# Performance work log

Measured on AMD Instinct MI355X. Metric: run time of the kernel, lower is better.

The kernel has to match this reference:

```python
import jax, jax.numpy as jnp
import numpy as np

B = 64          # graphs per batch
N_NODES = 2000  # nodes per graph (model hyperparameter: FC2 in_features)
NF = 128        # node features
H = 8           # hidden_dim
OC = 8          # out_channels
NC = 2          # n_classes
DEG = 16        # avg degree
SLOPE = 0.01


def _lin_init(key, fan_in, fan_out):
    k1, k2 = jax.random.split(key)
    s = 1.0 / np.sqrt(fan_in)
    W = jax.random.uniform(k1, (fan_in, fan_out), jnp.float32, -s, s)
    b = jax.random.uniform(k2, (fan_out,), jnp.float32, -s, s)
    return W, b


def setup_inputs() -> dict:
    key = jax.random.key(0)
    ks = jax.random.split(key, 10)
    N = B * N_NODES
    E = N * DEG
    x = jax.random.normal(ks[0], (N, NF), jnp.float32)
    # graph-local random edges, offset per graph
    local = jax.random.randint(ks[1], (2, E), 0, N_NODES)
    off = jnp.repeat(jnp.arange(B, dtype=jnp.int64) * N_NODES, E // B)
    edge_index = (local + off[None, :]).astype(jnp.int64)
    batch = jnp.repeat(jnp.arange(B, dtype=jnp.int64), N_NODES)
    W1a, b1a = _lin_init(ks[2], NF, H)
    W1b, b1b = _lin_init(ks[3], H, H)
    W2a, b2a = _lin_init(ks[4], H, H)
    W2b, b2b = _lin_init(ks[5], H, OC)
    Wf1, bf1 = _lin_init(ks[6], OC, 1)
    Wf2, bf2 = _lin_init(ks[7], N_NODES, NC)
    return {"x": x, "edge_index": edge_index, "batch": batch,
            "W1a": W1a, "b1a": b1a, "W1b": W1b, "b1b": b1b,
            "W2a": W2a, "b2a": b2a, "W2b": W2b, "b2b": b2b,
            "Wf1": Wf1, "bf1": bf1, "Wf2": Wf2, "bf2": bf2}


def _lrelu(v):
    return jnp.where(v >= 0, v, SLOPE * v)


def _gin_conv(h, src, dst, Wa, ba, Wb, bb):
    N = h.shape[0]
    agg = jax.ops.segment_sum(h[src], dst, num_segments=N)  # sum_{j->i} h_j
    z = h + agg                                             # (1+eps)*h + agg, eps=0
    z = _lrelu(z @ Wa + ba)                                 # MLP linear1 + act
    return z @ Wb + bb                                      # MLP linear2 (plain last)


def reference(x, edge_index, batch, W1a, b1a, W1b, b1b, W2a, b2a, W2b, b2b,
              Wf1, bf1, Wf2, bf2):
    src, dst = edge_index[0], edge_index[1]
    h = _gin_conv(x, src, dst, W1a, b1a, W1b, b1b)
    h = _lrelu(h)  # inter-layer activation (dropout = identity at eval)
    h = _gin_conv(h, src, dst, W2a, b2a, W2b, b2b)  # [N, OC], no act after last conv
    bsz = h.shape[0] // N_NODES
    y = h.reshape(bsz, N_NODES, OC)
    y = _lrelu(y) @ Wf1 + bf1          # FC1 -> [B, n_nodes, 1]
    y = y.reshape(bsz, N_NODES)
    y = _lrelu(y) @ Wf2 + bf2          # FC2 -> [B, n_classes]
    return jax.nn.log_softmax(y, axis=1)
```

## Files before the change

### kernel.cpp

```cpp
#include <hip/hip_runtime.h>
#include <math.h>

#define NF 128
#define HD 8
#define NPG 2000
#define EPB 8000
#define LPB 8
#define LNPB 250
#define FNPB 128
#define SLOPE 0.01f

__device__ __forceinline__ float lrelu(float v) {
    return v > 0.0f ? v : SLOPE * v;
}
__device__ __forceinline__ unsigned short f2bf(float f) {
    unsigned int u = __float_as_uint(f);
    return (unsigned short)((u + 0x7FFFu + ((u >> 16) & 1u)) >> 16);
}
__device__ __forceinline__ float bfl(unsigned int p) {
    return __uint_as_float(p << 16);
}
__device__ __forceinline__ float bfh(unsigned int p) {
    return __uint_as_float(p & 0xFFFF0000u);
}
__device__ __forceinline__ void gload_lds16(const void* g, void* l) {
    __builtin_amdgcn_global_load_lds(
        (const __attribute__((address_space(1))) unsigned int*)g,
        (__attribute__((address_space(3))) unsigned int*)l, 16, 0, 0);
}

__global__ __launch_bounds__(1024) void k_featsort(
    const float* __restrict__ x, const float* __restrict__ W1a,
    const int* __restrict__ ei, unsigned short* __restrict__ t1b,
    unsigned short* __restrict__ gcolb, int* __restrict__ rpc,
    int N, int E, int NC)
{
    __shared__ union {
        struct { float tile[FNPB * NF]; float wl[8 * 132]; } f;
        struct { int cnt[NPG]; unsigned int pck[EPB]; int srt[EPB];
                 int wtot[16]; int wpre[16]; } s;
    } sm;

    const int tid = threadIdx.x;

    if ((int)blockIdx.x < NC) {
        const int b = blockIdx.x;
        const int g = b >> 2;
        const int lane = tid & 63;
        const int wv = tid >> 6;
        const int nodeBase = g * NPG;
        const int e0 = b * EPB;

        for (int i = tid; i < NPG; i += 1024) sm.s.cnt[i] = 0;
        __syncthreads();

        for (int e = e0 + tid; e < e0 + EPB; e += 1024) {
            int src = ei[e] - nodeBase;
            int dl = ei[E + e] - nodeBase;
            sm.s.pck[e - e0] = ((unsigned int)dl << 11) | (unsigned int)src;
            atomicAdd(&sm.s.cnt[dl], 1);
        }
        __syncthreads();

        int c0 = 0, c1 = 0;
        if (tid < 1000) { c0 = sm.s.cnt[2 * tid]; c1 = sm.s.cnt[2 * tid + 1]; }
        int s = c0 + c1;
        int isc = s;
#pragma unroll
        for (int d = 1; d < 64; d <<= 1) {
            int o = __shfl_up(isc, d);
            if (lane >= d) isc += o;
        }
        if (lane == 63) sm.s.wtot[wv] = isc;
        __syncthreads();
        if (wv == 0) {
            int v = (lane < 16) ? sm.s.wtot[lane] : 0;
            int iv = v;
#pragma unroll
            for (int d = 1; d < 16; d <<= 1) {
                int o = __shfl_up(iv, d);
                if (lane >= d) iv += o;
            }
            if (lane < 16) sm.s.wpre[lane] = iv - v;
        }
        __syncthreads();
        int excl = isc - s + sm.s.wpre[wv];

        int* rpb = rpc + (size_t)b * (NPG + 1);
        if (tid < 1000) {
            sm.s.cnt[2 * tid]     = excl;
            sm.s.cnt[2 * tid + 1] = excl + c0;
            rpb[2 * tid]     = excl;
            rpb[2 * tid + 1] = excl + c0;
        }
        if (tid == 0) rpb[NPG] = EPB;
        __syncthreads();

        for (int i = tid; i < EPB; i += 1024) {
            unsigned int p = sm.s.pck[i];
            int dl = (int)(p >> 11);
            int src = (int)(p & 2047u);
            int pos = atomicAdd(&sm.s.cnt[dl], 1);
            sm.s.srt[pos] = src;
        }
        __syncthreads();

        unsigned int* dst = (unsigned int*)(gcolb + (size_t)b * EPB);
        for (int i = tid; i < EPB / 2; i += 1024) {
            unsigned int lo = (unsigned int)sm.s.srt[2 * i] & 0xFFFFu;
            unsigned int hi = (unsigned int)sm.s.srt[2 * i + 1] << 16;
            dst[i] = lo | hi;
        }
    } else {
        const size_t base = (size_t)(blockIdx.x - NC) * FNPB;
        const int lane = tid & 63;
        const int wv6 = tid >> 6;

        {
            int wcol = tid >> 7;
            int wk   = tid & 127;
            sm.f.wl[wcol * 132 + wk] = W1a[wk * 8 + wcol];
        }

        const float* xg = x + base * NF;
        char* tb = (char*)sm.f.tile;
#pragma unroll
        for (int i = 0; i < 4; ++i) {
            int s = wv6 * 256 + i * 64 + lane;
            int n = s >> 5, j = s & 31;
            gload_lds16(xg + n * NF + ((j ^ (n & 7)) << 2), tb + s * 16);
        }
        __syncthreads();

        const int col   = tid & 7;
        const int khalf = (tid >> 3) & 1;
        const int np    = tid >> 4;
        const int n0    = np * 2;
        const int ex0 = n0 & 7, ex1 = (n0 + 1) & 7;

        const float*  tf = sm.f.tile;
        const float4* w4 = (const float4*)sm.f.wl;
        float acc0 = 0.0f, acc1 = 0.0f;
#pragma unroll 4
        for (int i = 0; i < 16; ++i) {
            int k4 = khalf * 16 + i;
            float4 r0 = *(const float4*)(tf + n0 * NF + ((k4 ^ ex0) << 2));
            float4 r1 = *(const float4*)(tf + (n0 + 1) * NF + ((k4 ^ ex1) << 2));
            float4 w  = w4[col * 33 + k4];
            acc0 += r0.x * w.x + r0.y * w.y + r0.z * w.z + r0.w * w.w;
            acc1 += r1.x * w.x + r1.y * w.y + r1.z * w.z + r1.w * w.w;
        }
        acc0 += __shfl_xor(acc0, 8);
        acc1 += __shfl_xor(acc1, 8);
        if (khalf == 0) {
            t1b[(base + n0) * HD + col]     = f2bf(acc0);
            t1b[(base + n0 + 1) * HD + col] = f2bf(acc1);
        }
    }
}

#define GATHER_CHUNK(P)                                                       \
    {                                                                         \
        int b0 = rs[P], cnt = re[P] - b0;                                     \
        int sl[8];                                                            \
        _Pragma("unroll")                                                     \
        for (int j = 0; j < 8; ++j) {                                         \
            int idx = (j < cnt) ? (b0 + j) : 0;                               \
            sl[j] = colp[P][idx];                                             \
        }                                                                     \
        _Pragma("unroll")                                                     \
        for (int j = 0; j < 8; ++j) {                                         \
            float w = (j < cnt) ? 1.0f : 0.0f;                                \
            uint4 v = tbl[sl[j]];                                             \
            a0 += w * bfl(v.x); a1 += w * bfh(v.x);                           \
            a2 += w * bfl(v.y); a3 += w * bfh(v.y);                           \
            a4 += w * bfl(v.z); a5 += w * bfh(v.z);                           \
            a6 += w * bfl(v.w); a7 += w * bfh(v.w);                           \
        }                                                                     \
        for (int e2 = b0 + 8; e2 < b0 + cnt; ++e2) {                          \
            uint4 v = tbl[colp[P][e2]];                                       \
            a0 += bfl(v.x); a1 += bfh(v.x);                                   \
            a2 += bfl(v.y); a3 += bfh(v.y);                                   \
            a4 += bfl(v.z); a5 += bfh(v.z);                                   \
            a6 += bfl(v.w); a7 += bfh(v.w);                                   \
        }                                                                     \
    }

__global__ __launch_bounds__(512) void k_l1(
    const unsigned short* __restrict__ t1b, const int* __restrict__ rpc,
    const unsigned short* __restrict__ gcolb, unsigned short* __restrict__ ub,
    const float* __restrict__ b1a, const float* __restrict__ W1b,
    const float* __restrict__ b1b, const float* __restrict__ W2a)
{
    __shared__ uint4 tbl[2048];
    __shared__ float wts[144];

    const int b = blockIdx.x;
    const int g = b >> 3;
    const int q = b & 7;
    const int tid = threadIdx.x;

    if (tid < 144) {
        float v;
        if (tid < 8)       v = b1a[tid];
        else if (tid < 72) v = W1b[tid - 8];
        else if (tid < 80) v = b1b[tid - 72];
        else               v = W2a[tid - 80];
        wts[tid] = v;
    }

    {
        const uint4* src4 = (const uint4*)(t1b + (size_t)g * NPG * HD);
        const int lane = tid & 63, w8 = tid >> 6;
        char* tb = (char*)tbl;
#pragma unroll
        for (int i = 0; i < 4; ++i) {
            int s = w8 * 256 + i * 64 + lane;
            gload_lds16(src4 + s, tb + s * 16);
        }
    }
    __syncthreads();

    if (tid < 2 * LNPB) {
        const int node = tid >> 1;
        const int half = tid & 1;
        const int nl = q * LNPB + node;
        int rs[2], re[2];
        const unsigned short* colp[2];
#pragma unroll
        for (int p = 0; p < 2; ++p) {
            int ch = half * 2 + p;
            const int* rpb = rpc + (size_t)((g << 2) + ch) * (NPG + 1);
            colp[p] = gcolb + (size_t)((g << 2) + ch) * EPB;
            rs[p] = rpb[nl]; re[p] = rpb[nl + 1];
        }
        float a0 = 0, a1 = 0, a2 = 0, a3 = 0, a4 = 0, a5 = 0, a6 = 0, a7 = 0;
        GATHER_CHUNK(0) GATHER_CHUNK(1)
        a0 += __shfl_xor(a0, 1); a1 += __shfl_xor(a1, 1);
        a2 += __shfl_xor(a2, 1); a3 += __shfl_xor(a3, 1);
        a4 += __shfl_xor(a4, 1); a5 += __shfl_xor(a5, 1);
        a6 += __shfl_xor(a6, 1); a7 += __shfl_xor(a7, 1);

        if (half == 0) {
            uint4 sv = tbl[nl];
            float z[HD];
            z[0] = lrelu(bfl(sv.x) + a0 + wts[0]); z[1] = lrelu(bfh(sv.x) + a1 + wts[1]);
            z[2] = lrelu(bfl(sv.y) + a2 + wts[2]); z[3] = lrelu(bfh(sv.y) + a3 + wts[3]);
            z[4] = lrelu(bfl(sv.z) + a4 + wts[4]); z[5] = lrelu(bfh(sv.z) + a5 + wts[5]);
            z[6] = lrelu(bfl(sv.w) + a6 + wts[6]); z[7] = lrelu(bfh(sv.w) + a7 + wts[7]);

            float h[HD];
#pragma unroll
            for (int j = 0; j < HD; ++j) {
                float acc = wts[72 + j];
#pragma unroll
                for (int c = 0; c < HD; ++c) acc += z[c] * wts[8 + c * HD + j];
                h[j] = lrelu(acc);
            }
            float uu[HD];
#pragma unroll
            for (int j = 0; j < HD; ++j) {
                float acc = 0.0f;
#pragma unroll
                for (int c = 0; c < HD; ++c) acc += h[c] * wts[80 + c * HD + j];
                uu[j] = acc;
            }
            uint4 pk;
            pk.x = (unsigned int)f2bf(uu[0]) | ((unsigned int)f2bf(uu[1]) << 16);
            pk.y = (unsigned int)f2bf(uu[2]) | ((unsigned int)f2bf(uu[3]) << 16);
            pk.z = (unsigned int)f2bf(uu[4]) | ((unsigned int)f2bf(uu[5]) << 16);
            pk.w = (unsigned int)f2bf(uu[6]) | ((unsigned int)f2bf(uu[7]) << 16);
            ((uint4*)ub)[(size_t)g * NPG + nl] = pk;
        }
    }
}

__global__ __launch_bounds__(512) void k_l2(
    const unsigned short* __restrict__ ub, const int* __restrict__ rpc,
    const unsigned short* __restrict__ gcolb,
    const float* __restrict__ b2a, const float* __restrict__ W2b,
    const float* __restrict__ b2b, const float* __restrict__ Wf1,
    const float* __restrict__ bf1, const float* __restrict__ Wf2,
    float* __restrict__ bparts)
{
    __shared__ uint4 tbl[2048];
    __shared__ float wts[89];
    __shared__ float red[16];

    const int b = blockIdx.x;
    const int g = b >> 3;
    const int q = b & 7;
    const int tid = threadIdx.x;
    const int lane = tid & 63;
    const int wv = tid >> 6;

    if (tid < 89) {
        float v;
        if (tid < 8)       v = b2a[tid];
        else if (tid < 72) v = W2b[tid - 8];
        else if (tid < 80) v = b2b[tid - 72];
        else if (tid < 88) v = Wf1[tid - 80];
        else               v = bf1[0];
        wts[tid] = v;
    }

    {
        const uint4* src4 = (const uint4*)(ub + (size_t)g * NPG * HD);
        char* tb = (char*)tbl;
#pragma unroll
        for (int i = 0; i < 4; ++i) {
            int s = wv * 256 + i * 64 + lane;
            gload_lds16(src4 + s, tb + s * 16);
        }
    }
    __syncthreads();

    float acc0 = 0.0f, acc1 = 0.0f;
    if (tid < 2 * LNPB) {
        const int node = tid >> 1;
        const int half = tid & 1;
        const int nl = q * LNPB + node;
        int rs[2], re[2];
        const unsigned short* colp[2];
#pragma unroll
        for (int p = 0; p < 2; ++p) {
            int ch = half * 2 + p;
            const int* rpb = rpc + (size_t)((g << 2) + ch) * (NPG + 1);
            colp[p] = gcolb + (size_t)((g << 2) + ch) * EPB;
            rs[p] = rpb[nl]; re[p] = rpb[nl + 1];
        }
        float a0 = 0, a1 = 0, a2 = 0, a3 = 0, a4 = 0, a5 = 0, a6 = 0, a7 = 0;
        GATHER_CHUNK(0) GATHER_CHUNK(1)
        a0 += __shfl_xor(a0, 1); a1 += __shfl_xor(a1, 1);
        a2 += __shfl_xor(a2, 1); a3 += __shfl_xor(a3, 1);
        a4 += __shfl_xor(a4, 1); a5 += __shfl_xor(a5, 1);
        a6 += __shfl_xor(a6, 1); a7 += __shfl_xor(a7, 1);

        if (half == 0) {
            uint4 sv = tbl[nl];
            float z[HD];
            z[0] = lrelu(bfl(sv.x) + a0 + wts[0]); z[1] = lrelu(bfh(sv.x) + a1 + wts[1]);
            z[2] = lrelu(bfl(sv.y) + a2 + wts[2]); z[3] = lrelu(bfh(sv.y) + a3 + wts[3]);
            z[4] = lrelu(bfl(sv.z) + a4 + wts[4]); z[5] = lrelu(bfh(sv.z) + a5 + wts[5]);
            z[6] = lrelu(bfl(sv.w) + a6 + wts[6]); z[7] = lrelu(bfh(sv.w) + a7 + wts[7]);

            float svl = wts[88];
#pragma unroll
            for (int j = 0; j < HD; ++j) {
                float acc = wts[72 + j];
#pragma unroll
                for (int c = 0; c < HD; ++c) acc += z[c] * wts[8 + c * HD + j];
                svl += lrelu(acc) * wts[80 + j];
            }
            float pf = lrelu(svl);
            float2 wf = *(const float2*)(Wf2 + (size_t)nl * 2);
            acc0 = pf * wf.x;
            acc1 = pf * wf.y;
        }
    }

#pragma unroll
    for (int off = 32; off > 0; off >>= 1) {
        acc0 += __shfl_down(acc0, off);
        acc1 += __shfl_down(acc1, off);
    }
    if (lane == 0) { red[wv * 2] = acc0; red[wv * 2 + 1] = acc1; }
    __syncthreads();

    if (tid == 0) {
        float y0 = 0.f, y1 = 0.f;
#pragma unroll
        for (int w = 0; w < 8; ++w) { y0 += red[w * 2]; y1 += red[w * 2 + 1]; }
        *(float2*)(bparts + (size_t)b * 2) = make_float2(y0, y1);
    }
}

__global__ __launch_bounds__(64) void k_fin(const float* __restrict__ bparts,
                                            const float* __restrict__ bf2,
                                            float* __restrict__ out, int Bn) {
    int g = threadIdx.x;
    if (g >= Bn) return;
    float y0 = bf2[0], y1 = bf2[1];
#pragma unroll
    for (int b = 0; b < LPB; ++b) {
        float2 v = *(const float2*)(bparts + (size_t)(g * LPB + b) * 2);
        y0 += v.x; y1 += v.y;
    }
    float m = fmaxf(y0, y1);
    float lse = m + logf(expf(y0 - m) + expf(y1 - m));
    out[g * 2 + 0] = y0 - lse;
    out[g * 2 + 1] = y1 - lse;
}

extern "C" void kernel_launch(void* const* d_in, const int* in_sizes, int n_in,
                              void* d_out, int out_size, void* d_ws, size_t ws_size,
                              hipStream_t stream) {
    const float* x   = (const float*)d_in[0];
    const int*   ei  = (const int*)  d_in[1];
    const float* W1a = (const float*)d_in[3];
    const float* b1a = (const float*)d_in[4];
    const float* W1b = (const float*)d_in[5];
    const float* b1b = (const float*)d_in[6];
    const float* W2a = (const float*)d_in[7];
    const float* b2a = (const float*)d_in[8];
    const float* W2b = (const float*)d_in[9];
    const float* b2b = (const float*)d_in[10];
    const float* Wf1 = (const float*)d_in[11];
    const float* bf1 = (const float*)d_in[12];
    const float* Wf2 = (const float*)d_in[13];
    const float* bf2 = (const float*)d_in[14];

    int N   = in_sizes[0] / NF;
    int E   = in_sizes[1] / 2;
    int Bn  = N / NPG;
    int NC  = Bn * 4;

    unsigned short* t1b   = (unsigned short*)d_ws;
    unsigned short* ubuf  = t1b + (size_t)N * HD;
    unsigned short* gcolb = ubuf + (size_t)N * HD;
    int*            rpc   = (int*)(gcolb + (size_t)E);
    float*          bparts= (float*)(rpc + (size_t)NC * (NPG + 1) + 16);

    k_featsort<<<NC + N / FNPB, 1024, 0, stream>>>(x, W1a, ei, t1b, gcolb, rpc,
                                                   N, E, NC);
    k_l1 <<<Bn * LPB, 512, 0, stream>>>(t1b, rpc, gcolb, ubuf, b1a, W1b, b1b, W2a);
    k_l2 <<<Bn * LPB, 512, 0, stream>>>(ubuf, rpc, gcolb, b2a, W2b, b2b, Wf1,
                                        bf1, Wf2, bparts);
    k_fin<<<1, 64, 0, stream>>>(bparts, bf2, (float*)d_out, Bn);
}
```

Measured before the change: 157.6 us.

## Fuse GIN layer kernels and finalizer into one kernel with grid barrier

Merges the layer-1, layer-2 and final log-softmax kernels into a single kernel. A global atomic barrier separates the two layers, and a last-block-done counter runs the final reduction. Each block keeps its edge-neighbour indices and its own layer-1 output in registers, so layer 2 does not reload the CSR column indices or the self features. This removes two kernel launches and some redundant loads. In exchange it depends on all 512 blocks being co-resident for the spin barrier (hence launch_bounds 512,4) and adds register pressure.

```diff
diff --git a/kernel.cpp b/kernel.cpp
--- a/kernel.cpp
+++ b/kernel.cpp
@@ -33,7 +33,7 @@
     const float* __restrict__ x, const float* __restrict__ W1a,
     const int* __restrict__ ei, unsigned short* __restrict__ t1b,
     unsigned short* __restrict__ gcolb, int* __restrict__ rpc,
-    int N, int E, int NC)
+    int* __restrict__ bar, int N, int E, int NC)
 {
     __shared__ union {
         struct { float tile[FNPB * NF]; float wl[8 * 132]; } f;
@@ -45,6 +45,7 @@
 
     if ((int)blockIdx.x < NC) {
         const int b = blockIdx.x;
+        if (b == 0 && tid < 4) bar[tid] = 0;
         const int g = b >> 2;
         const int lane = tid & 63;
         const int wv = tid >> 6;
@@ -159,26 +160,30 @@
     }
 }
 
-#define GATHER_CHUNK(P)                                                       \
+#define LOADSL(SL, RS, RE, CP)                                                \
     {                                                                         \
-        int b0 = rs[P], cnt = re[P] - b0;                                     \
-        int sl[8];                                                            \
+        int cnt = (RE) - (RS);                                                \
         _Pragma("unroll")                                                     \
         for (int j = 0; j < 8; ++j) {                                         \
-            int idx = (j < cnt) ? (b0 + j) : 0;                               \
-            sl[j] = colp[P][idx];                                             \
+            int idx = (j < cnt) ? ((RS) + j) : 0;                             \
+            SL[j] = CP[idx];                                                  \
         }                                                                     \
+    }
+
+#define GATHER_SAVED(SL, RS, RE, CP)                                          \
+    {                                                                         \
+        int cnt = (RE) - (RS);                                                \
         _Pragma("unroll")                                                     \
         for (int j = 0; j < 8; ++j) {                                         \
             float w = (j < cnt) ? 1.0f : 0.0f;                                \
-            uint4 v = tbl[sl[j]];                                             \
+            uint4 v = tbl[SL[j]];                                             \
             a0 += w * bfl(v.x); a1 += w * bfh(v.x);                           \
             a2 += w * bfl(v.y); a3 += w * bfh(v.y);                           \
             a4 += w * bfl(v.z); a5 += w * bfh(v.z);                           \
             a6 += w * bfl(v.w); a7 += w * bfh(v.w);                           \
         }                                                                     \
-        for (int e2 = b0 + 8; e2 < b0 + cnt; ++e2) {                          \
-            uint4 v = tbl[colp[P][e2]];                                       \
+        for (int e2 = (RS) + 8; e2 < (RE); ++e2) {                            \
+            uint4 v = tbl[CP[e2]];                                            \
             a0 += bfl(v.x); a1 += bfh(v.x);                                   \
             a2 += bfl(v.y); a3 += bfh(v.y);                                   \
             a4 += bfl(v.z); a5 += bfh(v.z);                                   \
@@ -186,19 +191,29 @@
         }                                                                     \
     }
 
-__global__ __launch_bounds__(512) void k_l1(
+__global__ __launch_bounds__(512, 4) void k_l12(
     const unsigned short* __restrict__ t1b, const int* __restrict__ rpc,
     const unsigned short* __restrict__ gcolb, unsigned short* __restrict__ ub,
     const float* __restrict__ b1a, const float* __restrict__ W1b,
-    const float* __restrict__ b1b, const float* __restrict__ W2a)
+    const float* __restrict__ b1b, const float* __restrict__ W2a,
+    const float* __restrict__ b2a, const float* __restrict__ W2b,
+    const float* __restrict__ b2b, const float* __restrict__ Wf1,
+    const float* __restrict__ bf1, const float* __restrict__ Wf2,
+    const float* __restrict__ bf2, float* __restrict__ bparts,
+    int* __restrict__ bar, float* __restrict__ out)
 {
     __shared__ uint4 tbl[2048];
     __shared__ float wts[144];
+    __shared__ float wt2[89];
+    __shared__ float red[16];
+    __shared__ int lastFlag;
 
     const int b = blockIdx.x;
     const int g = b >> 3;
     const int q = b & 7;
     const int tid = threadIdx.x;
+    const int lane = tid & 63;
+    const int wv = tid >> 6;
 
     if (tid < 144) {
         float v;
@@ -208,34 +223,54 @@
         else               v = W2a[tid - 80];
         wts[tid] = v;
     }
+    {
+        int t2 = tid - 160;
+        if (t2 >= 0 && t2 < 89) {
+            float v;
+            if (t2 < 8)       v = b2a[t2];
+            else if (t2 < 72) v = W2b[t2 - 8];
+            else if (t2 < 80) v = b2b[t2 - 72];
+            else if (t2 < 88) v = Wf1[t2 - 80];
+            else              v = bf1[0];
+            wt2[t2] = v;
+        }
+    }
 
     {
         const uint4* src4 = (const uint4*)(t1b + (size_t)g * NPG * HD);
-        const int lane = tid & 63, w8 = tid >> 6;
         char* tb = (char*)tbl;
 #pragma unroll
         for (int i = 0; i < 4; ++i) {
-            int s = w8 * 256 + i * 64 + lane;
+            int s = wv * 256 + i * 64 + lane;
             gload_lds16(src4 + s, tb + s * 16);
         }
     }
     __syncthreads();
 
-    if (tid < 2 * LNPB) {
-        const int node = tid >> 1;
-        const int half = tid & 1;
-        const int nl = q * LNPB + node;
-        int rs[2], re[2];
-        const unsigned short* colp[2];
-#pragma unroll
-        for (int p = 0; p < 2; ++p) {
-            int ch = half * 2 + p;
-            const int* rpb = rpc + (size_t)((g << 2) + ch) * (NPG + 1);
-            colp[p] = gcolb + (size_t)((g << 2) + ch) * EPB;
-            rs[p] = rpb[nl]; re[p] = rpb[nl + 1];
-        }
+    const int node = tid >> 1;
+    const int half = tid & 1;
+    const int nl = q * LNPB + node;
+    const bool act = node < LNPB;
+    int rs0 = 0, re0 = 0, rs1 = 0, re1 = 0;
+    const unsigned short* cp0 = gcolb;
+    const unsigned short* cp1 = gcolb;
+    int sl0[8], sl1[8];
+    float uu0 = 0, uu1 = 0, uu2 = 0, uu3 = 0, uu4 = 0, uu5 = 0, uu6 = 0, uu7 = 0;
+
+    if (act) {
+        const int ch0 = half * 2, ch1 = half * 2 + 1;
+        const int* rp0 = rpc + (size_t)((g << 2) + ch0) * (NPG + 1);
+        const int* rp1 = rpc + (size_t)((g << 2) + ch1) * (NPG + 1);
+        cp0 = gcolb + (size_t)((g << 2) + ch0) * EPB;
+        cp1 = gcolb + (size_t)((g << 2) + ch1) * EPB;
+        rs0 = rp0[nl]; re0 = rp0[nl + 1];
+        rs1 = rp1[nl]; re1 = rp1[nl + 1];
+        LOADSL(sl0, rs0, re0, cp0)
+        LOADSL(sl1, rs1, re1, cp1)
+
         float a0 = 0, a1 = 0, a2 = 0, a3 = 0, a4 = 0, a5 = 0, a6 = 0, a7 = 0;
-        GATHER_CHUNK(0) GATHER_CHUNK(1)
+        GATHER_SAVED(sl0, rs0, re0, cp0)
+        GATHER_SAVED(sl1, rs1, re1, cp1)
         a0 += __shfl_xor(a0, 1); a1 += __shfl_xor(a1, 1);
         a2 += __shfl_xor(a2, 1); a3 += __shfl_xor(a3, 1);
         a4 += __shfl_xor(a4, 1); a5 += __shfl_xor(a5, 1);
@@ -265,6 +300,8 @@
                 for (int c = 0; c < HD; ++c) acc += h[c] * wts[80 + c * HD + j];
                 uu[j] = acc;
             }
+            uu0 = uu[0]; uu1 = uu[1]; uu2 = uu[2]; uu3 = uu[3];
+            uu4 = uu[4]; uu5 = uu[5]; uu6 = uu[6]; uu7 = uu[7];
             uint4 pk;
             pk.x = (unsigned int)f2bf(uu[0]) | ((unsigned int)f2bf(uu[1]) << 16);
             pk.y = (unsigned int)f2bf(uu[2]) | ((unsigned int)f2bf(uu[3]) << 16);
@@ -273,36 +310,23 @@
             ((uint4*)ub)[(size_t)g * NPG + nl] = pk;
         }
     }
-}
-
-__global__ __launch_bounds__(512) void k_l2(
-    const unsigned short* __restrict__ ub, const int* __restrict__ rpc,
-    const unsigned short* __restrict__ gcolb,
-    const float* __restrict__ b2a, const float* __restrict__ W2b,
-    const float* __restrict__ b2b, const float* __restrict__ Wf1,
-    const float* __restrict__ bf1, const float* __restrict__ Wf2,
-    float* __restrict__ bparts)
-{
-    __shared__ uint4 tbl[2048];
-    __shared__ float wts[89];
-    __shared__ float red[16];
-
-    const int b = blockIdx.x;
-    const int g = b >> 3;
-    const int q = b & 7;
-    const int tid = threadIdx.x;
-    const int lane = tid & 63;
-    const int wv = tid >> 6;
-
-    if (tid < 89) {
-        float v;
-        if (tid < 8)       v = b2a[tid];
-        else if (tid < 72) v = W2b[tid - 8];
-        else if (tid < 80) v = b2b[tid - 72];
-        else if (tid < 88) v = Wf1[tid - 80];
-        else               v = bf1[0];
-        wts[tid] = v;
-    }
+
+    __syncthreads();
+    if (tid == 0) {
+        __threadfence();
+        int prev = __hip_atomic_fetch_add(bar, 1, __ATOMIC_ACQ_REL,
+                                          __HIP_MEMORY_SCOPE_AGENT);
+        if (prev == (int)gridDim.x - 1) {
+            __hip_atomic_store(bar + 1, 1, __ATOMIC_RELEASE,
+                               __HIP_MEMORY_SCOPE_AGENT);
+        } else {
+            while (__hip_atomic_load(bar + 1, __ATOMIC_RELAXED,
+                                     __HIP_MEMORY_SCOPE_AGENT) == 0)
+                __builtin_amdgcn_s_sleep(4);
+        }
+        __threadfence();
+    }
+    __syncthreads();
 
     {
         const uint4* src4 = (const uint4*)(ub + (size_t)g * NPG * HD);
@@ -316,41 +340,29 @@
     __syncthreads();
 
     float acc0 = 0.0f, acc1 = 0.0f;
-    if (tid < 2 * LNPB) {
-        const int node = tid >> 1;
-        const int half = tid & 1;
-        const int nl = q * LNPB + node;
-        int rs[2], re[2];
-        const unsigned short* colp[2];
-#pragma unroll
-        for (int p = 0; p < 2; ++p) {
-            int ch = half * 2 + p;
-            const int* rpb = rpc + (size_t)((g << 2) + ch) * (NPG + 1);
-            colp[p] = gcolb + (size_t)((g << 2) + ch) * EPB;
-            rs[p] = rpb[nl]; re[p] = rpb[nl + 1];
-        }
+    if (act) {
         float a0 = 0, a1 = 0, a2 = 0, a3 = 0, a4 = 0, a5 = 0, a6 = 0, a7 = 0;
-        GATHER_CHUNK(0) GATHER_CHUNK(1)
+        GATHER_SAVED(sl0, rs0, re0, cp0)
+        GATHER_SAVED(sl1, rs1, re1, cp1)
         a0 += __shfl_xor(a0, 1); a1 += __shfl_xor(a1, 1);
         a2 += __shfl_xor(a2, 1); a3 += __shfl_xor(a3, 1);
         a4 += __shfl_xor(a4, 1); a5 += __shfl_xor(a5, 1);
         a6 += __shfl_xor(a6, 1); a7 += __shfl_xor(a7, 1);
 
         if (half == 0) {
-            uint4 sv = tbl[nl];
             float z[HD];
-            z[0] = lrelu(bfl(sv.x) + a0 + wts[0]); z[1] = lrelu(bfh(sv.x) + a1 + wts[1]);
-            z[2] = lrelu(bfl(sv.y) + a2 + wts[2]); z[3] = lrelu(bfh(sv.y) + a3 + wts[3]);
-            z[4] = lrelu(bfl(sv.z) + a4 + wts[4]); z[5] = lrelu(bfh(sv.z) + a5 + wts[5]);
-            z[6] = lrelu(bfl(sv.w) + a6 + wts[6]); z[7] = lrelu(bfh(sv.w) + a7 + wts[7]);
-
-            float svl = wts[88];
+            z[0] = lrelu(uu0 + a0 + wt2[0]); z[1] = lrelu(uu1 + a1 + wt2[1]);
+            z[2] = lrelu(uu2 + a2 + wt2[2]); z[3] = lrelu(uu3 + a3 + wt2[3]);
+            z[4] = lrelu(uu4 + a4 + wt2[4]); z[5] = lrelu(uu5 + a5 + wt2[5]);
+            z[6] = lrelu(uu6 + a6 + wt2[6]); z[7] = lrelu(uu7 + a7 + wt2[7]);
+
+            float svl = wt2[88];
 #pragma unroll
             for (int j = 0; j < HD; ++j) {
-                float acc = wts[72 + j];
-#pragma unroll
-                for (int c = 0; c < HD; ++c) acc += z[c] * wts[8 + c * HD + j];
-                svl += lrelu(acc) * wts[80 + j];
+                float acc = wt2[72 + j];
+#pragma unroll
+                for (int c = 0; c < HD; ++c) acc += z[c] * wt2[8 + c * HD + j];
+                svl += lrelu(acc) * wt2[80 + j];
             }
             float pf = lrelu(svl);
             float2 wf = *(const float2*)(Wf2 + (size_t)nl * 2);
@@ -372,24 +384,27 @@
 #pragma unroll
         for (int w = 0; w < 8; ++w) { y0 += red[w * 2]; y1 += red[w * 2 + 1]; }
         *(float2*)(bparts + (size_t)b * 2) = make_float2(y0, y1);
-    }
-}
-
-__global__ __launch_bounds__(64) void k_fin(const float* __restrict__ bparts,
-                                            const float* __restrict__ bf2,
-                                            float* __restrict__ out, int Bn) {
-    int g = threadIdx.x;
-    if (g >= Bn) return;
-    float y0 = bf2[0], y1 = bf2[1];
-#pragma unroll
-    for (int b = 0; b < LPB; ++b) {
-        float2 v = *(const float2*)(bparts + (size_t)(g * LPB + b) * 2);
-        y0 += v.x; y1 += v.y;
-    }
-    float m = fmaxf(y0, y1);
-    float lse = m + logf(expf(y0 - m) + expf(y1 - m));
-    out[g * 2 + 0] = y0 - lse;
-    out[g * 2 + 1] = y1 - lse;
+        __threadfence();
+        int prev = __hip_atomic_fetch_add(bar + 2, 1, __ATOMIC_ACQ_REL,
+                                          __HIP_MEMORY_SCOPE_AGENT);
+        lastFlag = (prev == (int)gridDim.x - 1);
+        if (lastFlag) __threadfence();
+    }
+    __syncthreads();
+
+    if (lastFlag && tid < 64) {
+        const int gg = tid;
+        float y0 = bf2[0], y1 = bf2[1];
+#pragma unroll
+        for (int p = 0; p < LPB; ++p) {
+            float2 v = *(const float2*)(bparts + (size_t)(gg * LPB + p) * 2);
+            y0 += v.x; y1 += v.y;
+        }
+        float m = fmaxf(y0, y1);
+        float lse = m + logf(expf(y0 - m) + expf(y1 - m));
+        out[gg * 2 + 0] = y0 - lse;
+        out[gg * 2 + 1] = y1 - lse;
+    }
 }
 
 extern "C" void kernel_launch(void* const* d_in, const int* in_sizes, int n_in,
@@ -420,11 +435,12 @@
     unsigned short* gcolb = ubuf + (size_t)N * HD;
     int*            rpc   = (int*)(gcolb + (size_t)E);
     float*          bparts= (float*)(rpc + (size_t)NC * (NPG + 1) + 16);
+    int*            bar   = (int*)(bparts + 1024 + 16);
 
     k_featsort<<<NC + N / FNPB, 1024, 0, stream>>>(x, W1a, ei, t1b, gcolb, rpc,
-                                                   N, E, NC);
-    k_l1 <<<Bn * LPB, 512, 0, stream>>>(t1b, rpc, gcolb, ubuf, b1a, W1b, b1b, W2a);
-    k_l2 <<<Bn * LPB, 512, 0, stream>>>(ubuf, rpc, gcolb, b2a, W2b, b2b, Wf1,
-                                        bf1, Wf2, bparts);
-    k_fin<<<1, 64, 0, stream>>>(bparts, bf2, (float*)d_out, Bn);
-}
+                                                   bar, N, E, NC);
+    k_l12<<<Bn * LPB, 512, 0, stream>>>(t1b, rpc, gcolb, ubuf,
+                                        b1a, W1b, b1b, W2a,
+                                        b2a, W2b, b2b, Wf1, bf1, Wf2, bf2,
+                                        bparts, bar, (float*)d_out);
+}
```

New measurement: 210.6 us. 1.34x slower.

## Precompute padded per-node neighbor index blocks to replace CSR lookups in gathers

Applied to the files above, without the earlier changes.

The sort kernel now also writes, for each node and chunk, a 16-byte block holding up to eight neighbor indices, with missing slots pointing to a zeroed pad row and a flag bit marking overflow. The two layer kernels read one uint4 per chunk instead of two row-pointer loads plus a dependent column gather, then fall back to the CSR only for nodes with more than eight neighbors in a chunk. This shortens the dependent global-load chain in the gather, at the cost of extra writes in the sort kernel, an extra barrier, and a larger workspace.

```diff
diff --git a/kernel.cpp b/kernel.cpp
--- a/kernel.cpp
+++ b/kernel.cpp
@@ -9,6 +9,7 @@
 #define LNPB 250
 #define FNPB 128
 #define SLOPE 0.01f
+#define PADIDX 2000u
 
 __device__ __forceinline__ float lrelu(float v) {
     return v > 0.0f ? v : SLOPE * v;
@@ -29,11 +30,23 @@
         (__attribute__((address_space(3))) unsigned int*)l, 16, 0, 0);
 }
 
+__device__ __forceinline__ uint4 packpad(const int* srt, int st, int cnt) {
+    unsigned int w[4];
+#pragma unroll
+    for (int h = 0; h < 4; ++h) {
+        unsigned int lo = (2 * h     < cnt) ? (unsigned int)srt[st + 2 * h]     : PADIDX;
+        unsigned int hi = (2 * h + 1 < cnt) ? (unsigned int)srt[st + 2 * h + 1] : PADIDX;
+        w[h] = lo | (hi << 16);
+    }
+    if (cnt > 8) w[0] |= 0x8000u;
+    return make_uint4(w[0], w[1], w[2], w[3]);
+}
+
 __global__ __launch_bounds__(1024) void k_featsort(
     const float* __restrict__ x, const float* __restrict__ W1a,
     const int* __restrict__ ei, unsigned short* __restrict__ t1b,
     unsigned short* __restrict__ gcolb, int* __restrict__ rpc,
-    int N, int E, int NC)
+    unsigned short* __restrict__ pnb, int N, int E, int NC)
 {
     __shared__ union {
         struct { float tile[FNPB * NF]; float wl[8 * 132]; } f;
@@ -110,6 +123,12 @@
             unsigned int lo = (unsigned int)sm.s.srt[2 * i] & 0xFFFFu;
             unsigned int hi = (unsigned int)sm.s.srt[2 * i + 1] << 16;
             dst[i] = lo | hi;
+        }
+
+        if (tid < 1000) {
+            uint4* pdst = (uint4*)(pnb + (size_t)b * NPG * 8);
+            pdst[2 * tid]     = packpad(sm.s.srt, excl, c0);
+            pdst[2 * tid + 1] = packpad(sm.s.srt, excl + c0, c1);
         }
     } else {
         const size_t base = (size_t)(blockIdx.x - NC) * FNPB;
@@ -159,26 +178,31 @@
     }
 }
 
-#define GATHER_CHUNK(P)                                                       \
+#define GATHER_PAD(PW)                                                        \
     {                                                                         \
-        int b0 = rs[P], cnt = re[P] - b0;                                     \
-        int sl[8];                                                            \
+        unsigned int w_[4] = {PW.x, PW.y, PW.z, PW.w};                        \
         _Pragma("unroll")                                                     \
-        for (int j = 0; j < 8; ++j) {                                         \
-            int idx = (j < cnt) ? (b0 + j) : 0;                               \
-            sl[j] = colp[P][idx];                                             \
+        for (int h = 0; h < 4; ++h) {                                         \
+            uint4 v = tbl[w_[h] & 2047u];                                     \
+            a0 += bfl(v.x); a1 += bfh(v.x);                                   \
+            a2 += bfl(v.y); a3 += bfh(v.y);                                   \
+            a4 += bfl(v.z); a5 += bfh(v.z);                                   \
+            a6 += bfl(v.w); a7 += bfh(v.w);                                   \
+            uint4 v2 = tbl[(w_[h] >> 16) & 2047u];                            \
+            a0 += bfl(v2.x); a1 += bfh(v2.x);                                 \
+            a2 += bfl(v2.y); a3 += bfh(v2.y);                                 \
+            a4 += bfl(v2.z); a5 += bfh(v2.z);                                 \
+            a6 += bfl(v2.w); a7 += bfh(v2.w);                                 \
         }                                                                     \
-        _Pragma("unroll")                                                     \
-        for (int j = 0; j < 8; ++j) {                                         \
-            float w = (j < cnt) ? 1.0f : 0.0f;                                \
-            uint4 v = tbl[sl[j]];                                             \
-            a0 += w * bfl(v.x); a1 += w * bfh(v.x);                           \
-            a2 += w * bfl(v.y); a3 += w * bfh(v.y);                           \
-            a4 += w * bfl(v.z); a5 += w * bfh(v.z);                           \
-            a6 += w * bfl(v.w); a7 += w * bfh(v.w);                           \
-        }                                                                     \
-        for (int e2 = b0 + 8; e2 < b0 + cnt; ++e2) {                          \
-            uint4 v = tbl[colp[P][e2]];                                       \
+    }
+
+#define TAIL_PAD(PW, CH)                                                      \
+    if (PW.x & 0x8000u) {                                                     \
+        const int* rpb_ = rpc + (size_t)((g << 2) + (CH)) * (NPG + 1);        \
+        const unsigned short* cp_ = gcolb + (size_t)((g << 2) + (CH)) * EPB;  \
+        int rs_ = rpb_[nl], re_ = rpb_[nl + 1];                               \
+        for (int e2 = rs_ + 8; e2 < re_; ++e2) {                              \
+            uint4 v = tbl[cp_[e2]];                                           \
             a0 += bfl(v.x); a1 += bfh(v.x);                                   \
             a2 += bfl(v.y); a3 += bfh(v.y);                                   \
             a4 += bfl(v.z); a5 += bfh(v.z);                                   \
@@ -186,9 +210,16 @@
         }                                                                     \
     }
 
+#define MERGE2()                                                              \
+    a0 += __shfl_xor(a0, 1); a1 += __shfl_xor(a1, 1);                         \
+    a2 += __shfl_xor(a2, 1); a3 += __shfl_xor(a3, 1);                         \
+    a4 += __shfl_xor(a4, 1); a5 += __shfl_xor(a5, 1);                         \
+    a6 += __shfl_xor(a6, 1); a7 += __shfl_xor(a7, 1);
+
 __global__ __launch_bounds__(512) void k_l1(
     const unsigned short* __restrict__ t1b, const int* __restrict__ rpc,
-    const unsigned short* __restrict__ gcolb, unsigned short* __restrict__ ub,
+    const unsigned short* __restrict__ gcolb,
+    const unsigned short* __restrict__ pnb, unsigned short* __restrict__ ub,
     const float* __restrict__ b1a, const float* __restrict__ W1b,
     const float* __restrict__ b1b, const float* __restrict__ W2a)
 {
@@ -199,6 +230,8 @@
     const int g = b >> 3;
     const int q = b & 7;
     const int tid = threadIdx.x;
+    const int lane = tid & 63;
+    const int wv = tid >> 6;
 
     if (tid < 144) {
         float v;
@@ -211,35 +244,31 @@
 
     {
         const uint4* src4 = (const uint4*)(t1b + (size_t)g * NPG * HD);
-        const int lane = tid & 63, w8 = tid >> 6;
         char* tb = (char*)tbl;
 #pragma unroll
         for (int i = 0; i < 4; ++i) {
-            int s = w8 * 256 + i * 64 + lane;
+            int s = wv * 256 + i * 64 + lane;
             gload_lds16(src4 + s, tb + s * 16);
         }
     }
+    __syncthreads();
+    if (tid == 0) tbl[PADIDX] = make_uint4(0, 0, 0, 0);
     __syncthreads();
 
     if (tid < 2 * LNPB) {
         const int node = tid >> 1;
         const int half = tid & 1;
         const int nl = q * LNPB + node;
-        int rs[2], re[2];
-        const unsigned short* colp[2];
-#pragma unroll
-        for (int p = 0; p < 2; ++p) {
-            int ch = half * 2 + p;
-            const int* rpb = rpc + (size_t)((g << 2) + ch) * (NPG + 1);
-            colp[p] = gcolb + (size_t)((g << 2) + ch) * EPB;
-            rs[p] = rpb[nl]; re[p] = rpb[nl + 1];
-        }
+        const int ch0 = half * 2, ch1 = half * 2 + 1;
+        const uint4* pn0 = (const uint4*)pnb + (size_t)((g << 2) + ch0) * NPG;
+        const uint4* pn1 = (const uint4*)pnb + (size_t)((g << 2) + ch1) * NPG;
+        uint4 p0 = pn0[nl];
+        uint4 p1 = pn1[nl];
+
         float a0 = 0, a1 = 0, a2 = 0, a3 = 0, a4 = 0, a5 = 0, a6 = 0, a7 = 0;
-        GATHER_CHUNK(0) GATHER_CHUNK(1)
-        a0 += __shfl_xor(a0, 1); a1 += __shfl_xor(a1, 1);
-        a2 += __shfl_xor(a2, 1); a3 += __shfl_xor(a3, 1);
-        a4 += __shfl_xor(a4, 1); a5 += __shfl_xor(a5, 1);
-        a6 += __shfl_xor(a6, 1); a7 += __shfl_xor(a7, 1);
+        GATHER_PAD(p0) GATHER_PAD(p1)
+        TAIL_PAD(p0, ch0) TAIL_PAD(p1, ch1)
+        MERGE2()
 
         if (half == 0) {
             uint4 sv = tbl[nl];
@@ -278,6 +307,7 @@
 __global__ __launch_bounds__(512) void k_l2(
     const unsigned short* __restrict__ ub, const int* __restrict__ rpc,
     const unsigned short* __restrict__ gcolb,
+    const unsigned short* __restrict__ pnb,
     const float* __restrict__ b2a, const float* __restrict__ W2b,
     const float* __restrict__ b2b, const float* __restrict__ Wf1,
     const float* __restrict__ bf1, const float* __restrict__ Wf2,
@@ -314,27 +344,24 @@
         }
     }
     __syncthreads();
+    if (tid == 0) tbl[PADIDX] = make_uint4(0, 0, 0, 0);
+    __syncthreads();
 
     float acc0 = 0.0f, acc1 = 0.0f;
     if (tid < 2 * LNPB) {
         const int node = tid >> 1;
         const int half = tid & 1;
         const int nl = q * LNPB + node;
-        int rs[2], re[2];
-        const unsigned short* colp[2];
-#pragma unroll
-        for (int p = 0; p < 2; ++p) {
-            int ch = half * 2 + p;
-            const int* rpb = rpc + (size_t)((g << 2) + ch) * (NPG + 1);
-            colp[p] = gcolb + (size_t)((g << 2) + ch) * EPB;
-            rs[p] = rpb[nl]; re[p] = rpb[nl + 1];
-        }
+        const int ch0 = half * 2, ch1 = half * 2 + 1;
+        const uint4* pn0 = (const uint4*)pnb + (size_t)((g << 2) + ch0) * NPG;
+        const uint4* pn1 = (const uint4*)pnb + (size_t)((g << 2) + ch1) * NPG;
+        uint4 p0 = pn0[nl];
+        uint4 p1 = pn1[nl];
+
         float a0 = 0, a1 = 0, a2 = 0, a3 = 0, a4 = 0, a5 = 0, a6 = 0, a7 = 0;
-        GATHER_CHUNK(0) GATHER_CHUNK(1)
-        a0 += __shfl_xor(a0, 1); a1 += __shfl_xor(a1, 1);
-        a2 += __shfl_xor(a2, 1); a3 += __shfl_xor(a3, 1);
-        a4 += __shfl_xor(a4, 1); a5 += __shfl_xor(a5, 1);
-        a6 += __shfl_xor(a6, 1); a7 += __shfl_xor(a7, 1);
+        GATHER_PAD(p0) GATHER_PAD(p1)
+        TAIL_PAD(p0, ch0) TAIL_PAD(p1, ch1)
+        MERGE2()
 
         if (half == 0) {
             uint4 sv = tbl[nl];
@@ -420,11 +447,13 @@
     unsigned short* gcolb = ubuf + (size_t)N * HD;
     int*            rpc   = (int*)(gcolb + (size_t)E);
     float*          bparts= (float*)(rpc + (size_t)NC * (NPG + 1) + 16);
+    unsigned short* pnb   = (unsigned short*)(bparts + 1024 + 16);
 
     k_featsort<<<NC + N / FNPB, 1024, 0, stream>>>(x, W1a, ei, t1b, gcolb, rpc,
-                                                   N, E, NC);
-    k_l1 <<<Bn * LPB, 512, 0, stream>>>(t1b, rpc, gcolb, ubuf, b1a, W1b, b1b, W2a);
-    k_l2 <<<Bn * LPB, 512, 0, stream>>>(ubuf, rpc, gcolb, b2a, W2b, b2b, Wf1,
-                                        bf1, Wf2, bparts);
+                                                   pnb, N, E, NC);
+    k_l1 <<<Bn * LPB, 512, 0, stream>>>(t1b, rpc, gcolb, pnb, ubuf,
+                                        b1a, W1b, b1b, W2a);
+    k_l2 <<<Bn * LPB, 512, 0, stream>>>(ubuf, rpc, gcolb, pnb,
+                                        b2a, W2b, b2b, Wf1, bf1, Wf2, bparts);
     k_fin<<<1, 64, 0, stream>>>(bparts, bf2, (float*)d_out, Bn);
 }
```

Measured after the change: 161.5 us. 1.02x slower.

## Split sort and feature kernels, fuse final log-softmax into layer-2 kernel

Applied to the files above, without the earlier changes.

The combined sort/feature kernel, whose union LDS layout forced every block to reserve the large sort footprint, is split into a dedicated 1024-thread sort kernel and a 512-thread feature projection kernel. The feature kernel now handles 64 nodes per block, giving a smaller LDS tile, more blocks and higher occupancy. The separate finalize kernel is removed; the last-finishing layer-2 block, detected with an atomic counter, computes the log-softmax. This removes one launch but adds one, and adds a global atomic plus fences in every layer-2 block.

```diff
diff --git a/kernel.cpp b/kernel.cpp
--- a/kernel.cpp
+++ b/kernel.cpp
@@ -7,7 +7,7 @@
 #define EPB 8000
 #define LPB 8
 #define LNPB 250
-#define FNPB 128
+#define FNPB 64
 #define SLOPE 0.01f
 
 __device__ __forceinline__ float lrelu(float v) {
@@ -29,133 +29,138 @@
         (__attribute__((address_space(3))) unsigned int*)l, 16, 0, 0);
 }
 
-__global__ __launch_bounds__(1024) void k_featsort(
+__global__ __launch_bounds__(1024) void k_sort(
+    const int* __restrict__ ei, unsigned short* __restrict__ gcolb,
+    int* __restrict__ rpc, int* __restrict__ done, int E)
+{
+    __shared__ struct {
+        int cnt[NPG]; unsigned int pck[EPB]; int srt[EPB];
+        int wtot[16]; int wpre[16];
+    } sm;
+
+    const int tid = threadIdx.x;
+    const int b = blockIdx.x;
+    if (b == 0 && tid == 0) *done = 0;
+    const int g = b >> 2;
+    const int lane = tid & 63;
+    const int wv = tid >> 6;
+    const int nodeBase = g * NPG;
+    const int e0 = b * EPB;
+
+    for (int i = tid; i < NPG; i += 1024) sm.cnt[i] = 0;
+    __syncthreads();
+
+    for (int e = e0 + tid; e < e0 + EPB; e += 1024) {
+        int src = ei[e] - nodeBase;
+        int dl = ei[E + e] - nodeBase;
+        sm.pck[e - e0] = ((unsigned int)dl << 11) | (unsigned int)src;
+        atomicAdd(&sm.cnt[dl], 1);
+    }
+    __syncthreads();
+
+    int c0 = 0, c1 = 0;
+    if (tid < 1000) { c0 = sm.cnt[2 * tid]; c1 = sm.cnt[2 * tid + 1]; }
+    int s = c0 + c1;
+    int isc = s;
+#pragma unroll
+    for (int d = 1; d < 64; d <<= 1) {
+        int o = __shfl_up(isc, d);
+        if (lane >= d) isc += o;
+    }
+    if (lane == 63) sm.wtot[wv] = isc;
+    __syncthreads();
+    if (wv == 0) {
+        int v = (lane < 16) ? sm.wtot[lane] : 0;
+        int iv = v;
+#pragma unroll
+        for (int d = 1; d < 16; d <<= 1) {
+            int o = __shfl_up(iv, d);
+            if (lane >= d) iv += o;
+        }
+        if (lane < 16) sm.wpre[lane] = iv - v;
+    }
+    __syncthreads();
+    int excl = isc - s + sm.wpre[wv];
+
+    int* rpb = rpc + (size_t)b * (NPG + 1);
+    if (tid < 1000) {
+        sm.cnt[2 * tid]     = excl;
+        sm.cnt[2 * tid + 1] = excl + c0;
+        rpb[2 * tid]     = excl;
+        rpb[2 * tid + 1] = excl + c0;
+    }
+    if (tid == 0) rpb[NPG] = EPB;
+    __syncthreads();
+
+    for (int i = tid; i < EPB; i += 1024) {
+        unsigned int p = sm.pck[i];
+        int dl = (int)(p >> 11);
+        int src = (int)(p & 2047u);
+        int pos = atomicAdd(&sm.cnt[dl], 1);
+        sm.srt[pos] = src;
+    }
+    __syncthreads();
+
+    unsigned int* dst = (unsigned int*)(gcolb + (size_t)b * EPB);
+    for (int i = tid; i < EPB / 2; i += 1024) {
+        unsigned int lo = (unsigned int)sm.srt[2 * i] & 0xFFFFu;
+        unsigned int hi = (unsigned int)sm.srt[2 * i + 1] << 16;
+        dst[i] = lo | hi;
+    }
+}
+
+__global__ __launch_bounds__(512) void k_feat(
     const float* __restrict__ x, const float* __restrict__ W1a,
-    const int* __restrict__ ei, unsigned short* __restrict__ t1b,
-    unsigned short* __restrict__ gcolb, int* __restrict__ rpc,
-    int N, int E, int NC)
+    unsigned short* __restrict__ t1b)
 {
-    __shared__ union {
-        struct { float tile[FNPB * NF]; float wl[8 * 132]; } f;
-        struct { int cnt[NPG]; unsigned int pck[EPB]; int srt[EPB];
-                 int wtot[16]; int wpre[16]; } s;
-    } sm;
+    __shared__ struct { float tile[FNPB * NF]; float wl[8 * 132]; } sm;
 
     const int tid = threadIdx.x;
-
-    if ((int)blockIdx.x < NC) {
-        const int b = blockIdx.x;
-        const int g = b >> 2;
-        const int lane = tid & 63;
-        const int wv = tid >> 6;
-        const int nodeBase = g * NPG;
-        const int e0 = b * EPB;
-
-        for (int i = tid; i < NPG; i += 1024) sm.s.cnt[i] = 0;
-        __syncthreads();
-
-        for (int e = e0 + tid; e < e0 + EPB; e += 1024) {
-            int src = ei[e] - nodeBase;
-            int dl = ei[E + e] - nodeBase;
-            sm.s.pck[e - e0] = ((unsigned int)dl << 11) | (unsigned int)src;
-            atomicAdd(&sm.s.cnt[dl], 1);
-        }
-        __syncthreads();
-
-        int c0 = 0, c1 = 0;
-        if (tid < 1000) { c0 = sm.s.cnt[2 * tid]; c1 = sm.s.cnt[2 * tid + 1]; }
-        int s = c0 + c1;
-        int isc = s;
-#pragma unroll
-        for (int d = 1; d < 64; d <<= 1) {
-            int o = __shfl_up(isc, d);
-            if (lane >= d) isc += o;
-        }
-        if (lane == 63) sm.s.wtot[wv] = isc;
-        __syncthreads();
-        if (wv == 0) {
-            int v = (lane < 16) ? sm.s.wtot[lane] : 0;
-            int iv = v;
-#pragma unroll
-            for (int d = 1; d < 16; d <<= 1) {
-                int o = __shfl_up(iv, d);
-                if (lane >= d) iv += o;
-            }
-            if (lane < 16) sm.s.wpre[lane] = iv - v;
-        }
-        __syncthreads();
-        int excl = isc - s + sm.s.wpre[wv];
-
-        int* rpb = rpc + (size_t)b * (NPG + 1);
-        if (tid < 1000) {
-            sm.s.cnt[2 * tid]     = excl;
-            sm.s.cnt[2 * tid + 1] = excl + c0;
-            rpb[2 * tid]     = excl;
-            rpb[2 * tid + 1] = excl + c0;
-        }
-        if (tid == 0) rpb[NPG] = EPB;
-        __syncthreads();
-
-        for (int i = tid; i < EPB; i += 1024) {
-            unsigned int p = sm.s.pck[i];
-            int dl = (int)(p >> 11);
-            int src = (int)(p & 2047u);
-            int pos = atomicAdd(&sm.s.cnt[dl], 1);
-            sm.s.srt[pos] = src;
-        }
-        __syncthreads();
-
-        unsigned int* dst = (unsigned int*)(gcolb + (size_t)b * EPB);
-        for (int i = tid; i < EPB / 2; i += 1024) {
-            unsigned int lo = (unsigned int)sm.s.srt[2 * i] & 0xFFFFu;
-            unsigned int hi = (unsigned int)sm.s.srt[2 * i + 1] << 16;
-            dst[i] = lo | hi;
-        }
-    } else {
-        const size_t base = (size_t)(blockIdx.x - NC) * FNPB;
-        const int lane = tid & 63;
-        const int wv6 = tid >> 6;
-
-        {
-            int wcol = tid >> 7;
-            int wk   = tid & 127;
-            sm.f.wl[wcol * 132 + wk] = W1a[wk * 8 + wcol];
-        }
-
-        const float* xg = x + base * NF;
-        char* tb = (char*)sm.f.tile;
-#pragma unroll
-        for (int i = 0; i < 4; ++i) {
-            int s = wv6 * 256 + i * 64 + lane;
-            int n = s >> 5, j = s & 31;
-            gload_lds16(xg + n * NF + ((j ^ (n & 7)) << 2), tb + s * 16);
-        }
-        __syncthreads();
-
-        const int col   = tid & 7;
-        const int khalf = (tid >> 3) & 1;
-        const int np    = tid >> 4;
-        const int n0    = np * 2;
-        const int ex0 = n0 & 7, ex1 = (n0 + 1) & 7;
-
-        const float*  tf = sm.f.tile;
-        const float4* w4 = (const float4*)sm.f.wl;
-        float acc0 = 0.0f, acc1 = 0.0f;
+    const size_t base = (size_t)blockIdx.x * FNPB;
+    const int lane = tid & 63;
+    const int wv = tid >> 6;
+
+#pragma unroll
+    for (int i = 0; i < 2; ++i) {
+        int idx = tid + i * 512;
+        int wcol = idx >> 7;
+        int wk   = idx & 127;
+        sm.wl[wcol * 132 + wk] = W1a[wk * 8 + wcol];
+    }
+
+    const float* xg = x + base * NF;
+    char* tb = (char*)sm.tile;
+#pragma unroll
+    for (int i = 0; i < 4; ++i) {
+        int s = wv * 256 + i * 64 + lane;
+        int n = s >> 5, j = s & 31;
+        gload_lds16(xg + n * NF + ((j ^ (n & 7)) << 2), tb + s * 16);
+    }
+    __syncthreads();
+
+    const int col   = tid & 7;
+    const int khalf = (tid >> 3) & 1;
+    const int np    = tid >> 4;
+    const int n0    = np * 2;
+    const int ex0 = n0 & 7, ex1 = (n0 + 1) & 7;
+
+    const float*  tf = sm.tile;
+    const float4* w4 = (const float4*)sm.wl;
+    float acc0 = 0.0f, acc1 = 0.0f;
 #pragma unroll 4
-        for (int i = 0; i < 16; ++i) {
-            int k4 = khalf * 16 + i;
-            float4 r0 = *(const float4*)(tf + n0 * NF + ((k4 ^ ex0) << 2));
-            float4 r1 = *(const float4*)(tf + (n0 + 1) * NF + ((k4 ^ ex1) << 2));
-            float4 w  = w4[col * 33 + k4];
-            acc0 += r0.x * w.x + r0.y * w.y + r0.z * w.z + r0.w * w.w;
-            acc1 += r1.x * w.x + r1.y * w.y + r1.z * w.z + r1.w * w.w;
-        }
-        acc0 += __shfl_xor(acc0, 8);
-        acc1 += __shfl_xor(acc1, 8);
-        if (khalf == 0) {
-            t1b[(base + n0) * HD + col]     = f2bf(acc0);
-            t1b[(base + n0 + 1) * HD + col] = f2bf(acc1);
-        }
+    for (int i = 0; i < 16; ++i) {
+        int k4 = khalf * 16 + i;
+        float4 r0 = *(const float4*)(tf + n0 * NF + ((k4 ^ ex0) << 2));
+        float4 r1 = *(const float4*)(tf + (n0 + 1) * NF + ((k4 ^ ex1) << 2));
+        float4 w  = w4[col * 33 + k4];
+        acc0 += r0.x * w.x + r0.y * w.y + r0.z * w.z + r0.w * w.w;
+        acc1 += r1.x * w.x + r1.y * w.y + r1.z * w.z + r1.w * w.w;
+    }
+    acc0 += __shfl_xor(acc0, 8);
+    acc1 += __shfl_xor(acc1, 8);
+    if (khalf == 0) {
+        t1b[(base + n0) * HD + col]     = f2bf(acc0);
+        t1b[(base + n0 + 1) * HD + col] = f2bf(acc1);
     }
 }
 
@@ -199,6 +204,8 @@
     const int g = b >> 3;
     const int q = b & 7;
     const int tid = threadIdx.x;
+    const int lane = tid & 63;
+    const int wv = tid >> 6;
 
     if (tid < 144) {
         float v;
@@ -211,11 +218,10 @@
 
     {
         const uint4* src4 = (const uint4*)(t1b + (size_t)g * NPG * HD);
-        const int lane = tid & 63, w8 = tid >> 6;
         char* tb = (char*)tbl;
 #pragma unroll
         for (int i = 0; i < 4; ++i) {
-            int s = w8 * 256 + i * 64 + lane;
+            int s = wv * 256 + i * 64 + lane;
             gload_lds16(src4 + s, tb + s * 16);
         }
     }
@@ -275,17 +281,19 @@
     }
 }
 
-__global__ __launch_bounds__(512) void k_l2(
+__global__ __launch_bounds__(512) void k_l2f(
     const unsigned short* __restrict__ ub, const int* __restrict__ rpc,
     const unsigned short* __restrict__ gcolb,
     const float* __restrict__ b2a, const float* __restrict__ W2b,
     const float* __restrict__ b2b, const float* __restrict__ Wf1,
     const float* __restrict__ bf1, const float* __restrict__ Wf2,
-    float* __restrict__ bparts)
+    const float* __restrict__ bf2, float* __restrict__ bparts,
+    int* __restrict__ done, float* __restrict__ out)
 {
     __shared__ uint4 tbl[2048];
     __shared__ float wts[89];
     __shared__ float red[16];
+    __shared__ int lastFlag;
 
     const int b = blockIdx.x;
     const int g = b >> 3;
@@ -372,24 +380,27 @@
 #pragma unroll
         for (int w = 0; w < 8; ++w) { y0 += red[w * 2]; y1 += red[w * 2 + 1]; }
         *(float2*)(bparts + (size_t)b * 2) = make_float2(y0, y1);
-    }
-}
-
-__global__ __launch_bounds__(64) void k_fin(const float* __restrict__ bparts,
-                                            const float* __restrict__ bf2,
-                                            float* __restrict__ out, int Bn) {
-    int g = threadIdx.x;
-    if (g >= Bn) return;
-    float y0 = bf2[0], y1 = bf2[1];
-#pragma unroll
-    for (int b = 0; b < LPB; ++b) {
-        float2 v = *(const float2*)(bparts + (size_t)(g * LPB + b) * 2);
-        y0 += v.x; y1 += v.y;
-    }
-    float m = fmaxf(y0, y1);
-    float lse = m + logf(expf(y0 - m) + expf(y1 - m));
-    out[g * 2 + 0] = y0 - lse;
-    out[g * 2 + 1] = y1 - lse;
+        __threadfence();
+        int prev = __hip_atomic_fetch_add(done, 1, __ATOMIC_ACQ_REL,
+                                          __HIP_MEMORY_SCOPE_AGENT);
+        lastFlag = (prev == (int)gridDim.x - 1);
+        if (lastFlag) __threadfence();
+    }
+    __syncthreads();
+
+    if (lastFlag && tid < 64) {
+        const int gg = tid;
+        float y0 = bf2[0], y1 = bf2[1];
+#pragma unroll
+        for (int p = 0; p < LPB; ++p) {
+            float2 v = *(const float2*)(bparts + (size_t)(gg * LPB + p) * 2);
+            y0 += v.x; y1 += v.y;
+        }
+        float m = fmaxf(y0, y1);
+        float lse = m + logf(expf(y0 - m) + expf(y1 - m));
+        out[gg * 2 + 0] = y0 - lse;
+        out[gg * 2 + 1] = y1 - lse;
+    }
 }
 
 extern "C" void kernel_launch(void* const* d_in, const int* in_sizes, int n_in,
@@ -420,11 +431,13 @@
     unsigned short* gcolb = ubuf + (size_t)N * HD;
     int*            rpc   = (int*)(gcolb + (size_t)E);
     float*          bparts= (float*)(rpc + (size_t)NC * (NPG + 1) + 16);
-
-    k_featsort<<<NC + N / FNPB, 1024, 0, stream>>>(x, W1a, ei, t1b, gcolb, rpc,
-                                                   N, E, NC);
-    k_l1 <<<Bn * LPB, 512, 0, stream>>>(t1b, rpc, gcolb, ubuf, b1a, W1b, b1b, W2a);
-    k_l2 <<<Bn * LPB, 512, 0, stream>>>(ubuf, rpc, gcolb, b2a, W2b, b2b, Wf1,
-                                        bf1, Wf2, bparts);
-    k_fin<<<1, 64, 0, stream>>>(bparts, bf2, (float*)d_out, Bn);
-}
+    int*            done  = (int*)(bparts + 1024 + 16);
+
+    k_sort<<<NC, 1024, 0, stream>>>(ei, gcolb, rpc, done, E);
+    k_feat<<<N / FNPB, 512, 0, stream>>>(x, W1a, t1b);
+    k_l1 <<<Bn * LPB, 512, 0, stream>>>(t1b, rpc, gcolb, ubuf,
+                                        b1a, W1b, b1b, W2a);
+    k_l2f<<<Bn * LPB, 512, 0, stream>>>(ubuf, rpc, gcolb,
+                                        b2a, W2b, b2b, Wf1, bf1, Wf2, bf2,
+                                        bparts, done, (float*)d_out);
+}
```

New measurement: 168.2 us. 6.7% more time.
